# Performance work log

Measured on AMD Instinct MI355X. Metric: run time of the kernel, lower is better.

## Reference

```python
import jax, jax.numpy as jnp
import numpy as np

HID = 512


def _lstm_cell(x, h, c, W_ih, W_hh, b):
    # torch gate order: i, f, g, o ; z: [B, 4H]
    z = x @ W_ih.T + h @ W_hh.T + b
    i, f, g, o = jnp.split(z, 4, axis=-1)
    c_new = jax.nn.sigmoid(f) * c + jax.nn.sigmoid(i) * jnp.tanh(g)
    h_new = jax.nn.sigmoid(o) * jnp.tanh(c_new)
    return h_new, c_new


def setup_inputs() -> dict:
    key = jax.random.key(0)
    ks = jax.random.split(key, 10)
    s = 1.0 / np.sqrt(HID)  # torch default LSTM init scale
    return {
        "inputs": jax.random.normal(ks[0], (512, 512, 1), jnp.float32),
        "targets": jax.random.normal(ks[1], (512, 128, 1), jnp.float32),
        "enc_Wih": jax.random.uniform(ks[2], (4 * HID, 1), jnp.float32, -s, s),
        "enc_Whh": jax.random.uniform(ks[3], (4 * HID, HID), jnp.float32, -s, s),
        "enc_b": jax.random.uniform(ks[4], (4 * HID,), jnp.float32, -s, s),
        "dec_Wih": jax.random.uniform(ks[5], (4 * HID, 1), jnp.float32, -s, s),
        "dec_Whh": jax.random.uniform(ks[6], (4 * HID, HID), jnp.float32, -s, s),
        "dec_b": jax.random.uniform(ks[7], (4 * HID,), jnp.float32, -s, s),
        "lin_W": jax.random.uniform(ks[8], (1, HID), jnp.float32, -s, s),
        "lin_b": jax.random.uniform(ks[9], (1,), jnp.float32, -s, s),
        "target_len": 128,
        "teacher_forcing_ratio": 0,
    }


def reference(inputs, targets, enc_Wih, enc_Whh, enc_b,
              dec_Wih, dec_Whh, dec_b, lin_W, lin_b,
              target_len, teacher_forcing_ratio):
    B = inputs.shape[0]
    H = enc_Whh.shape[1]
    h0 = jnp.zeros((B, H), inputs.dtype)
    c0 = jnp.zeros((B, H), inputs.dtype)

    # ---- encoder: scan over source timesteps ----
    def enc_step(carry, x_t):  # x_t: [B, 1]
        h, c = carry
        h, c = _lstm_cell(x_t, h, c, enc_Wih, enc_Whh, enc_b)
        return (h, c), None

    (h, c), _ = jax.lax.scan(enc_step, (h0, c0), jnp.swapaxes(inputs, 0, 1))

    x0 = inputs[:, -1, :]  # [B, 1]

    def dec_step(carry, _):
        h, c, x = carry
        h, c = _lstm_cell(x, h, c, dec_Wih, dec_Whh, dec_b)
        out = h @ lin_W.T + lin_b  # [B, 1]
        return (h, c, out), out

    _, outs = jax.lax.scan(dec_step, (h, c, x0), None, length=target_len)
    return jnp.swapaxes(outs, 0, 1)  # [B, target_len, 1]
```

## Files before the change

### kernel.cpp

```cpp
#include <hip/hip_runtime.h>
#include <math.h>

#define HID    512
#define BATCH  512
#define TIN    512
#define TOUT   128
#define FOUR_H 2048
#define STEPS  (TIN + TOUT)

typedef __bf16 bf16x8 __attribute__((ext_vector_type(8)));
typedef float floatx4 __attribute__((ext_vector_type(4)));
typedef int   int4v   __attribute__((ext_vector_type(4)));

#define GLOADX4_SC(dst, p) \
    asm volatile("global_load_dwordx4 %0, %1, off sc0 sc1" : "=v"(dst) : "v"(p))
#define GSTOREX4_SC(p, v) \
    asm volatile("global_store_dwordx4 %0, %1, off sc0 sc1" :: "v"(p), "v"(v) : "memory")
#define GLOADX4_C(dst, p) \
    asm volatile("global_load_dwordx4 %0, %1, off" : "=v"(dst) : "v"(p))
#define WAIT_T1(N, r) asm volatile("s_waitcnt vmcnt(" #N ")" : "+v"(r))
#define WAIT_T4(N, B) asm volatile("s_waitcnt vmcnt(" #N ")" \
    : "+v"((B)[0]), "+v"((B)[1]), "+v"((B)[2]), "+v"((B)[3]))

__device__ __forceinline__ float fsig(float x) {
    return __builtin_amdgcn_rcpf(1.0f + __expf(-x));
}
__device__ __forceinline__ float ftanh(float x) {
    return 1.0f - 2.0f * __builtin_amdgcn_rcpf(1.0f + __expf(2.0f * x));
}

__global__ __launch_bounds__(256) void pack_w(
    const float* __restrict__ W, __bf16* __restrict__ Apk)
{
    int tid = blockIdx.x * 256 + threadIdx.x;
    int mp  = tid >> 6;
    int kg  = tid & 63;
    int g   = mp & 3;
    int j   = mp >> 2;
    int r   = g * HID + j;
    int blk   = mp >> 7;
    int rg    = (mp >> 4) & 7;
    int lr    = mp & 15;
    int chunk = kg >> 2;
    int lq    = kg & 3;
    int lane  = lq * 16 + lr;
    const float* src = W + (size_t)r * HID + kg * 8;
    size_t offHi = ((size_t)(((blk * 8 + rg) * 16 + chunk) * 2 + 0) * 512) + lane * 8;
    size_t offLo = ((size_t)(((blk * 8 + rg) * 16 + chunk) * 2 + 1) * 512) + lane * 8;
    __bf16 hibuf[8], lobuf[8];
    #pragma unroll
    for (int i = 0; i < 8; ++i) {
        float x = src[i];
        __bf16 hi = (__bf16)x;
        hibuf[i] = hi;
        lobuf[i] = (__bf16)(x - (float)hi);
    }
    *(bf16x8*)(Apk + offHi) = *(bf16x8*)hibuf;
    *(bf16x8*)(Apk + offLo) = *(bf16x8*)lobuf;
}

__global__ __launch_bounds__(256) void pack_v(
    const float* __restrict__ Wih, const float* __restrict__ b,
    float* __restrict__ WihP, float* __restrict__ bP)
{
    int mp = blockIdx.x * 256 + threadIdx.x;
    int g  = mp & 3;
    int j  = mp >> 2;
    int r  = g * HID + j;
    WihP[mp] = Wih[r];
    bP[mp]   = b[r];
}

__global__ __launch_bounds__(256) void transpose_in(
    const float* __restrict__ in, float* __restrict__ outT)
{
    int idx = blockIdx.x * 256 + threadIdx.x;
    int t = idx >> 9, b = idx & 511;
    outT[idx] = in[(size_t)b * TIN + t];
}

__global__ __launch_bounds__(256, 1) void lstm_persistent(
    const __bf16* __restrict__ ApkEnc,
    const __bf16* __restrict__ ApkDec,
    const float* __restrict__ WihPenc, const float* __restrict__ biasPenc,
    const float* __restrict__ WihPdec, const float* __restrict__ biasPdec,
    const float* __restrict__ inputsT,
    const float* __restrict__ linW, const float* __restrict__ linb,
    __bf16* __restrict__ h0,
    __bf16* __restrict__ h1,
    __bf16* __restrict__ h2,
    float* __restrict__ xacc,
    int* __restrict__ barrier_ws,
    float* __restrict__ out)
{
    extern __shared__ char smem[];
    __bf16* Alds   = (__bf16*)smem;
    char*   Bring  = smem + 131072;
    __bf16* hstage = (__bf16*)(smem + 147456);
    float*  xred   = (float*)(smem + 152576);

    const int tid  = threadIdx.x;
    const int lane = tid & 63;
    const int w    = tid >> 6;
    const int lr   = lane & 15;
    const int lq   = lane >> 4;
    const int by   = blockIdx.x >> 4;
    const int blk  = blockIdx.x & 15;
    const int nbase = by * 32;
    const int rgbase = 2 * w;
    const bool STREAM = (w >= 2);

    int* flagv = barrier_ws;

    const int m0a = blk * 128 + (rgbase + 0) * 16 + lq * 4;
    const int m0b = blk * 128 + (rgbase + 1) * 16 + lq * 4;
    const floatx4 wihE[2] = { *(const floatx4*)(WihPenc + m0a), *(const floatx4*)(WihPenc + m0b) };
    const floatx4 bE[2]   = { *(const floatx4*)(biasPenc + m0a), *(const floatx4*)(biasPenc + m0b) };
    const floatx4 wihD[2] = { *(const floatx4*)(WihPdec + m0a), *(const floatx4*)(WihPdec + m0b) };
    const floatx4 bD[2]   = { *(const floatx4*)(biasPdec + m0a), *(const floatx4*)(biasPdec + m0b) };
    const float lw[2] = { linW[m0a >> 2], linW[m0b >> 2] };
    const float lb = linb[0];

    int bn[2];
    #pragma unroll
    for (int nt = 0; nt < 2; ++nt) bn[nt] = nbase + nt * 16 + lr;

    {
        float* hz = (float*)hstage;
        for (int i = tid; i < 1280; i += 256) hz[i] = 0.f;
    }
    {
        const int4v* srcp = (const int4v*)(ApkEnc + (size_t)blk * 131072);
        int4v* dstp = (int4v*)Alds;
        for (int i = tid; i < 8192; i += 256) dstp[i] = srcp[i];
    }
    __syncthreads();

    float creg[2][2] = {{0.f, 0.f}, {0.f, 0.f}};

    __bf16* hA = h0;
    __bf16* hB = h1;
    __bf16* hC = h2;

    for (int s = 0; s < STEPS; ++s) {
        const bool dec = (s >= TIN);
        const int  t   = s - TIN;
        const __bf16* Acur = dec ? ApkDec : ApkEnc;

        if (s == TIN) {
            const int4v* srcp = (const int4v*)(ApkDec + (size_t)blk * 131072);
            int4v* dstp = (int4v*)Alds;
            for (int i = tid; i < 8192; i += 256) dstp[i] = srcp[i];
            __syncthreads();
        }

        const __bf16* srcB = hA + (size_t)by * 32768 + tid * 8;
        __bf16*       hout = hB;
        const __bf16* Ag   = Acur + (size_t)blk * 131072;

        float xq[2];
        if (!dec) {
            #pragma unroll
            for (int nt = 0; nt < 2; ++nt)
                xq[nt] = inputsT[s * BATCH + bn[nt]];
            asm volatile("" ::: "memory");
        }

        int4v st[4];
        int4v areg[2][4];
        if (STREAM) {
            #pragma unroll
            for (int mb = 0; mb < 2; ++mb)
                #pragma unroll
                for (int pl = 0; pl < 2; ++pl)
                    GLOADX4_C(areg[0][mb * 2 + pl],
                              Ag + (size_t)((((rgbase + mb) * 16 + blk) * 2 + pl) * 512) + lane * 8);
            #pragma unroll
            for (int mb = 0; mb < 2; ++mb)
                #pragma unroll
                for (int pl = 0; pl < 2; ++pl)
                    GLOADX4_C(areg[1][mb * 2 + pl],
                              Ag + (size_t)((((rgbase + mb) * 16 + ((blk + 1) & 15)) * 2 + pl) * 512) + lane * 8);
        }

        if (tid < 16) {
            const int* fp = &flagv[by * 16 + tid];
            while (__hip_atomic_load(fp, __ATOMIC_RELAXED, __HIP_MEMORY_SCOPE_AGENT) < s) {
                __builtin_amdgcn_s_sleep(1);
            }
        }

        floatx4 acc[2][2];
        #pragma unroll
        for (int mb = 0; mb < 2; ++mb)
            #pragma unroll
            for (int nt = 0; nt < 2; ++nt) acc[mb][nt] = floatx4{0.f, 0.f, 0.f, 0.f};

        {
            bf16x8 ah[2], al[2];
            if (STREAM) {
                WAIT_T4(4, areg[0]);
                #pragma unroll
                for (int mb = 0; mb < 2; ++mb) {
                    ah[mb] = __builtin_bit_cast(bf16x8, areg[0][mb * 2 + 0]);
                    al[mb] = __builtin_bit_cast(bf16x8, areg[0][mb * 2 + 1]);
                }
            } else {
                #pragma unroll
                for (int mb = 0; mb < 2; ++mb) {
                    const char* ap = (const char*)Alds
                        + (((rgbase + mb) * 16 + blk) * 2) * 1024 + lane * 16;
                    ah[mb] = *(const bf16x8*)(ap);
                    al[mb] = *(const bf16x8*)(ap + 1024);
                }
            }
            const char* hb = (const char*)hstage;
            const int kq = lane >> 4, lrp = lane & 15;
            bf16x8 bh0 = *(const bf16x8*)(hb + (     lrp) * 80 + kq * 16);
            bf16x8 bl0 = *(const bf16x8*)(hb + (32 + lrp) * 80 + kq * 16);
            bf16x8 bh1 = *(const bf16x8*)(hb + (16 + lrp) * 80 + kq * 16);
            bf16x8 bl1 = *(const bf16x8*)(hb + (48 + lrp) * 80 + kq * 16);
            #pragma unroll
            for (int mb = 0; mb < 2; ++mb) {
                acc[mb][0] = __builtin_amdgcn_mfma_f32_16x16x32_bf16(ah[mb], bh0, acc[mb][0], 0, 0, 0);
                acc[mb][1] = __builtin_amdgcn_mfma_f32_16x16x32_bf16(ah[mb], bh1, acc[mb][1], 0, 0, 0);
                acc[mb][0] = __builtin_amdgcn_mfma_f32_16x16x32_bf16(al[mb], bh0, acc[mb][0], 0, 0, 0);
                acc[mb][1] = __builtin_amdgcn_mfma_f32_16x16x32_bf16(al[mb], bh1, acc[mb][1], 0, 0, 0);
                acc[mb][0] = __builtin_amdgcn_mfma_f32_16x16x32_bf16(ah[mb], bl0, acc[mb][0], 0, 0, 0);
                acc[mb][1] = __builtin_amdgcn_mfma_f32_16x16x32_bf16(ah[mb], bl1, acc[mb][1], 0, 0, 0);
            }
        }

        __syncthreads();

        if (dec) {
            if (tid < 32) xred[tid] = 0.f;
            if (blk == 0) {
                if (t >= 1 && tid < 32) {
                    float v = __hip_atomic_load(&xacc[((t - 1) % 3) * BATCH + nbase + tid],
                                                __ATOMIC_RELAXED, __HIP_MEMORY_SCOPE_AGENT) + lb;
                    out[(size_t)(nbase + tid) * TOUT + (t - 1)] = v;
                }
                if (tid >= 32 && tid < 64) {
                    __hip_atomic_store(&xacc[((t + 1) % 3) * BATCH + nbase + (tid - 32)], 0.0f,
                                       __ATOMIC_RELAXED, __HIP_MEMORY_SCOPE_AGENT);
                }
            }
            #pragma unroll
            for (int nt = 0; nt < 2; ++nt)
                xq[nt] = (t == 0) ? inputsT[(TIN - 1) * BATCH + bn[nt]]
                                  : __hip_atomic_load(&xacc[((t - 1) % 3) * BATCH + bn[nt]],
                                                      __ATOMIC_RELAXED, __HIP_MEMORY_SCOPE_AGENT) + lb;
            asm volatile("" ::: "memory");
        }

        GLOADX4_SC(st[1], srcB + (size_t)((blk + 1) & 15) * 2048);
        GLOADX4_SC(st[2], srcB + (size_t)((blk + 2) & 15) * 2048);
        GLOADX4_SC(st[3], srcB + (size_t)((blk + 3) & 15) * 2048);

        #pragma unroll
        for (int it = 1; it < 16; ++it) {
            const int c = (blk + it) & 15;

            if (STREAM) {
                if      (it == 1)  { WAIT_T1(2,  st[it & 3]); }
                else if (it == 2)  { WAIT_T1(6,  st[it & 3]); }
                else if (it <= 13) { WAIT_T1(10, st[it & 3]); }
                else if (it == 14) { WAIT_T1(9,  st[it & 3]); }
                else               { WAIT_T1(8,  st[it & 3]); }
            } else {
                if      (it <= 13) { WAIT_T1(2, st[it & 3]); }
                else if (it == 14) { WAIT_T1(1, st[it & 3]); }
                else               { WAIT_T1(0, st[it & 3]); }
            }
            *(int4v*)(Bring + (it & 3) * 4096 + tid * 16) = st[it & 3];

            if (STREAM && it + 1 < 16) {
                const int cn = (blk + it + 1) & 15;
                #pragma unroll
                for (int mb = 0; mb < 2; ++mb)
                    #pragma unroll
                    for (int pl = 0; pl < 2; ++pl)
                        GLOADX4_C(areg[(it + 1) & 1][mb * 2 + pl],
                                  Ag + (size_t)((((rgbase + mb) * 16 + cn) * 2 + pl) * 512) + lane * 8);
            }
            if (it + 3 < 16)
                GLOADX4_SC(st[(it + 3) & 3], srcB + (size_t)((blk + it + 3) & 15) * 2048);

            __syncthreads();

            bf16x8 ah[2], al[2];
            if (STREAM) {
                if      (it == 1)  { WAIT_T4(7, areg[1]); }
                else if (it <= 12) { WAIT_T4(6, areg[it & 1]); }
                else if (it == 13) { WAIT_T4(5, areg[1]); }
                else if (it == 14) { WAIT_T4(4, areg[0]); }
                else               { WAIT_T4(0, areg[1]); }
                #pragma unroll
                for (int mb = 0; mb < 2; ++mb) {
                    ah[mb] = __builtin_bit_cast(bf16x8, areg[it & 1][mb * 2 + 0]);
                    al[mb] = __builtin_bit_cast(bf16x8, areg[it & 1][mb * 2 + 1]);
                }
            } else {
                #pragma unroll
                for (int mb = 0; mb < 2; ++mb) {
                    const char* ap = (const char*)Alds
                        + (((rgbase + mb) * 16 + c) * 2) * 1024 + lane * 16;
                    ah[mb] = *(const bf16x8*)(ap);
                    al[mb] = *(const bf16x8*)(ap + 1024);
                }
            }

            const char* bs = Bring + (it & 3) * 4096;
            bf16x8 bh0 = *(const bf16x8*)(bs + (0 * 128 + 0 * 64 + lane) * 16);
            bf16x8 bl0 = *(const bf16x8*)(bs + (0 * 128 + 1 * 64 + lane) * 16);
            bf16x8 bh1 = *(const bf16x8*)(bs + (1 * 128 + 0 * 64 + lane) * 16);
            bf16x8 bl1 = *(const bf16x8*)(bs + (1 * 128 + 1 * 64 + lane) * 16);

            #pragma unroll
            for (int mb = 0; mb < 2; ++mb) {
                acc[mb][0] = __builtin_amdgcn_mfma_f32_16x16x32_bf16(ah[mb], bh0, acc[mb][0], 0, 0, 0);
                acc[mb][1] = __builtin_amdgcn_mfma_f32_16x16x32_bf16(ah[mb], bh1, acc[mb][1], 0, 0, 0);
                acc[mb][0] = __builtin_amdgcn_mfma_f32_16x16x32_bf16(al[mb], bh0, acc[mb][0], 0, 0, 0);
                acc[mb][1] = __builtin_amdgcn_mfma_f32_16x16x32_bf16(al[mb], bh1, acc[mb][1], 0, 0, 0);
                acc[mb][0] = __builtin_amdgcn_mfma_f32_16x16x32_bf16(ah[mb], bl0, acc[mb][0], 0, 0, 0);
                acc[mb][1] = __builtin_amdgcn_mfma_f32_16x16x32_bf16(ah[mb], bl1, acc[mb][1], 0, 0, 0);
            }
        }

        const floatx4* wih = dec ? wihD : wihE;
        const floatx4* bb  = dec ? bD   : bE;
        float px[2] = {0.f, 0.f};
        #pragma unroll
        for (int mb = 0; mb < 2; ++mb) {
            const int jlocal = (rgbase + mb) * 4 + lq;
            #pragma unroll
            for (int nt = 0; nt < 2; ++nt) {
                float x  = xq[nt];
                float i_ = fsig (acc[mb][nt][0] + bb[mb][0] + x * wih[mb][0]);
                float f_ = fsig (acc[mb][nt][1] + bb[mb][1] + x * wih[mb][1]);
                float g_ = ftanh(acc[mb][nt][2] + bb[mb][2] + x * wih[mb][2]);
                float o_ = fsig (acc[mb][nt][3] + bb[mb][3] + x * wih[mb][3]);
                float cv = f_ * creg[mb][nt] + i_ * g_;
                creg[mb][nt] = cv;
                float h  = o_ * ftanh(cv);
                __bf16 hh = (__bf16)h;
                int bl = nt * 16 + lr;
                hstage[bl * 40 + jlocal] = hh;
                hstage[(32 + bl) * 40 + jlocal] = (__bf16)(h - (float)hh);
                if (dec) {
                    float v = h * lw[mb];
                    px[nt] += v;
                }
            }
        }
        if (dec) {
            #pragma unroll
            for (int nt = 0; nt < 2; ++nt) {
                px[nt] += __shfl_xor(px[nt], 16);
                px[nt] += __shfl_xor(px[nt], 32);
            }
        }

        __syncthreads();

        {
            int nt = tid >> 7, pl = (tid >> 6) & 1, ln = tid & 63;
            int kq = ln >> 4, lrp = ln & 15;
            const char* src = (const char*)hstage + (pl * 32 + nt * 16 + lrp) * 80 + kq * 16;
            int4v v = *(const int4v*)src;
            __bf16* dst = hout + (size_t)by * 32768 + blk * 2048 + tid * 8;
            GSTOREX4_SC(dst, v);
        }

        if (dec && lane < 16) {
            #pragma unroll
            for (int nt = 0; nt < 2; ++nt) atomicAdd(&xred[nt * 16 + lr], px[nt]);
        }
        __syncthreads();
        if (dec && tid < 32) {
            atomicAdd(&xacc[(t % 3) * BATCH + nbase + tid], xred[tid]);
        }

        __builtin_amdgcn_s_waitcnt(0);
        __syncthreads();
        if (tid == 0) {
            __hip_atomic_store(&flagv[by * 16 + blk], s + 1,
                               __ATOMIC_RELAXED, __HIP_MEMORY_SCOPE_AGENT);
        }

        __bf16* htmp = hA; hA = hB; hB = hC; hC = htmp;
    }

    if (blk == 0) {
        if (tid < 16) {
            const int* fp = &flagv[by * 16 + tid];
            while (__hip_atomic_load(fp, __ATOMIC_RELAXED, __HIP_MEMORY_SCOPE_AGENT) < STEPS) {
                __builtin_amdgcn_s_sleep(1);
            }
        }
        __syncthreads();
        if (tid < 32) {
            float v = __hip_atomic_load(&xacc[((TOUT - 1) % 3) * BATCH + nbase + tid],
                                        __ATOMIC_RELAXED, __HIP_MEMORY_SCOPE_AGENT) + lb;
            out[(size_t)(nbase + tid) * TOUT + (TOUT - 1)] = v;
        }
    }
}

extern "C" void kernel_launch(void* const* d_in, const int* in_sizes, int n_in,
                              void* d_out, int out_size, void* d_ws, size_t ws_size,
                              hipStream_t stream) {
    const float* inputs  = (const float*)d_in[0];
    const float* enc_Wih = (const float*)d_in[2];
    const float* enc_Whh = (const float*)d_in[3];
    const float* enc_b   = (const float*)d_in[4];
    const float* dec_Wih = (const float*)d_in[5];
    const float* dec_Whh = (const float*)d_in[6];
    const float* dec_b   = (const float*)d_in[7];
    const float* lin_W   = (const float*)d_in[8];
    const float* lin_b   = (const float*)d_in[9];
    float* out = (float*)d_out;

    char* ws = (char*)d_ws;
    const size_t SZ_APK = (size_t)FOUR_H * HID * 2 * sizeof(__bf16);
    const size_t SZ_V   = (size_t)FOUR_H * sizeof(float);
    const size_t SZ_HF  = (size_t)16 * 16 * 256 * 8 * sizeof(__bf16);

    __bf16* ApkEnc = (__bf16*)(ws);
    __bf16* ApkDec = (__bf16*)(ws + SZ_APK);
    char* p = ws + 2 * SZ_APK;
    float* WihPenc  = (float*)p;  p += SZ_V;
    float* biasPenc = (float*)p;  p += SZ_V;
    float* WihPdec  = (float*)p;  p += SZ_V;
    float* biasPdec = (float*)p;  p += SZ_V;
    float* inputsT  = (float*)p;  p += (size_t)TIN * BATCH * sizeof(float);
    __bf16* h0 = (__bf16*)p;      p += SZ_HF;
    __bf16* h1 = (__bf16*)p;      p += SZ_HF;
    __bf16* h2 = (__bf16*)p;      p += SZ_HF;
    float* xacc  = (float*)p;     p += 3 * BATCH * sizeof(float);
    int* barrier_ws = (int*)p;    p += 1024 * sizeof(int);

    pack_w<<<512, 256, 0, stream>>>(enc_Whh, ApkEnc);
    pack_w<<<512, 256, 0, stream>>>(dec_Whh, ApkDec);
    pack_v<<<8, 256, 0, stream>>>(enc_Wih, enc_b, WihPenc, biasPenc);
    pack_v<<<8, 256, 0, stream>>>(dec_Wih, dec_b, WihPdec, biasPdec);
    transpose_in<<<1024, 256, 0, stream>>>(inputs, inputsT);
    hipMemsetAsync(h0, 0, SZ_HF, stream);
    hipMemsetAsync(xacc, 0, 3 * BATCH * sizeof(float), stream);
    hipMemsetAsync(barrier_ws, 0, 1024 * sizeof(int), stream);

    const int shmem = 131072 + 16384 + 5120 + 128;
    hipFuncSetAttribute((const void*)lstm_persistent,
                        hipFuncAttributeMaxDynamicSharedMemorySize, shmem);

    void* args[] = {
        (void*)&ApkEnc, (void*)&ApkDec,
        (void*)&WihPenc, (void*)&biasPenc, (void*)&WihPdec, (void*)&biasPdec,
        (void*)&inputsT, (void*)&lin_W, (void*)&lin_b,
        (void*)&h0, (void*)&h1, (void*)&h2,
        (void*)&xacc, (void*)&barrier_ws, (void*)&out
    };
    hipLaunchCooperativeKernel((void*)lstm_persistent, dim3(256), dim3(256),
                               args, shmem, stream);
}
```

Measured before the change: 5.013 ms.

## Replace per-block flags with counter barrier and prefetch next step's local MFMA

Replaces the per-block step flags (each block waiting on 16 peers' flags) with a single arrive counter per batch group that blocks increment and then spin on. The first chunk of the next step's matrix product, which uses the block's own hidden-state slice already in LDS, is now computed before waiting on the barrier, so it overlaps the wait. The hidden-state buffers drop from triple to double buffering. Double buffering relies on the full barrier for write-after-read safety, and the simplified vmcnt waits must stay correct for the changed load order.

Result: faster. 4.200 ms (-16.2%).

```diff
diff --git a/kernel.cpp b/kernel.cpp
--- a/kernel.cpp
+++ b/kernel.cpp
@@ -88,7 +88,6 @@
     const float* __restrict__ linW, const float* __restrict__ linb,
     __bf16* __restrict__ h0,
     __bf16* __restrict__ h1,
-    __bf16* __restrict__ h2,
     float* __restrict__ xacc,
     int* __restrict__ barrier_ws,
     float* __restrict__ out)
@@ -110,7 +109,7 @@
     const int rgbase = 2 * w;
     const bool STREAM = (w >= 2);
 
-    int* flagv = barrier_ws;
+    int* arrive = barrier_ws + by * 32;
 
     const int m0a = blk * 128 + (rgbase + 0) * 16 + lq * 4;
     const int m0b = blk * 128 + (rgbase + 1) * 16 + lq * 4;
@@ -135,104 +134,77 @@
         for (int i = tid; i < 8192; i += 256) dstp[i] = srcp[i];
     }
     __syncthreads();
+    __builtin_amdgcn_s_waitcnt(0);
 
     float creg[2][2] = {{0.f, 0.f}, {0.f, 0.f}};
 
-    __bf16* hA = h0;
-    __bf16* hB = h1;
-    __bf16* hC = h2;
+    floatx4 acc[2][2];
+    int4v areg[2][4];
+
+    {
+        const __bf16* AgN = ApkEnc + (size_t)blk * 131072;
+        #pragma unroll
+        for (int mb = 0; mb < 2; ++mb)
+            #pragma unroll
+            for (int nt = 0; nt < 2; ++nt) acc[mb][nt] = floatx4{0.f, 0.f, 0.f, 0.f};
+        if (STREAM) {
+            #pragma unroll
+            for (int mb = 0; mb < 2; ++mb)
+                #pragma unroll
+                for (int pl = 0; pl < 2; ++pl)
+                    GLOADX4_C(areg[0][mb * 2 + pl],
+                              AgN + (size_t)((((rgbase + mb) * 16 + blk) * 2 + pl) * 512) + lane * 8);
+            #pragma unroll
+            for (int mb = 0; mb < 2; ++mb)
+                #pragma unroll
+                for (int pl = 0; pl < 2; ++pl)
+                    GLOADX4_C(areg[1][mb * 2 + pl],
+                              AgN + (size_t)((((rgbase + mb) * 16 + ((blk + 1) & 15)) * 2 + pl) * 512) + lane * 8);
+            WAIT_T4(4, areg[0]);
+        }
+        bf16x8 ah[2], al[2];
+        if (STREAM) {
+            #pragma unroll
+            for (int mb = 0; mb < 2; ++mb) {
+                ah[mb] = __builtin_bit_cast(bf16x8, areg[0][mb * 2 + 0]);
+                al[mb] = __builtin_bit_cast(bf16x8, areg[0][mb * 2 + 1]);
+            }
+        } else {
+            #pragma unroll
+            for (int mb = 0; mb < 2; ++mb) {
+                const char* ap = (const char*)Alds + (((rgbase + mb) * 16 + blk) * 2) * 1024 + lane * 16;
+                ah[mb] = *(const bf16x8*)(ap);
+                al[mb] = *(const bf16x8*)(ap + 1024);
+            }
+        }
+        const char* hb = (const char*)hstage;
+        const int kq = lane >> 4, lrp = lane & 15;
+        bf16x8 bh0 = *(const bf16x8*)(hb + (     lrp) * 80 + kq * 16);
+        bf16x8 bl0 = *(const bf16x8*)(hb + (32 + lrp) * 80 + kq * 16);
+        bf16x8 bh1 = *(const bf16x8*)(hb + (16 + lrp) * 80 + kq * 16);
+        bf16x8 bl1 = *(const bf16x8*)(hb + (48 + lrp) * 80 + kq * 16);
+        #pragma unroll
+        for (int mb = 0; mb < 2; ++mb) {
+            acc[mb][0] = __builtin_amdgcn_mfma_f32_16x16x32_bf16(ah[mb], bh0, acc[mb][0], 0, 0, 0);
+            acc[mb][1] = __builtin_amdgcn_mfma_f32_16x16x32_bf16(ah[mb], bh1, acc[mb][1], 0, 0, 0);
+            acc[mb][0] = __builtin_amdgcn_mfma_f32_16x16x32_bf16(al[mb], bh0, acc[mb][0], 0, 0, 0);
+            acc[mb][1] = __builtin_amdgcn_mfma_f32_16x16x32_bf16(al[mb], bh1, acc[mb][1], 0, 0, 0);
+            acc[mb][0] = __builtin_amdgcn_mfma_f32_16x16x32_bf16(ah[mb], bl0, acc[mb][0], 0, 0, 0);
+            acc[mb][1] = __builtin_amdgcn_mfma_f32_16x16x32_bf16(ah[mb], bl1, acc[mb][1], 0, 0, 0);
+        }
+    }
 
     for (int s = 0; s < STEPS; ++s) {
         const bool dec = (s >= TIN);
         const int  t   = s - TIN;
         const __bf16* Acur = dec ? ApkDec : ApkEnc;
 
-        if (s == TIN) {
-            const int4v* srcp = (const int4v*)(ApkDec + (size_t)blk * 131072);
-            int4v* dstp = (int4v*)Alds;
-            for (int i = tid; i < 8192; i += 256) dstp[i] = srcp[i];
-            __syncthreads();
-        }
-
-        const __bf16* srcB = hA + (size_t)by * 32768 + tid * 8;
-        __bf16*       hout = hB;
+        const __bf16* hin  = (s & 1) ? h1 : h0;
+        __bf16*       hout = (s & 1) ? h0 : h1;
+        const __bf16* srcB = hin + (size_t)by * 32768 + tid * 8;
         const __bf16* Ag   = Acur + (size_t)blk * 131072;
 
         float xq[2];
-        if (!dec) {
-            #pragma unroll
-            for (int nt = 0; nt < 2; ++nt)
-                xq[nt] = inputsT[s * BATCH + bn[nt]];
-            asm volatile("" ::: "memory");
-        }
-
-        int4v st[4];
-        int4v areg[2][4];
-        if (STREAM) {
-            #pragma unroll
-            for (int mb = 0; mb < 2; ++mb)
-                #pragma unroll
-                for (int pl = 0; pl < 2; ++pl)
-                    GLOADX4_C(areg[0][mb * 2 + pl],
-                              Ag + (size_t)((((rgbase + mb) * 16 + blk) * 2 + pl) * 512) + lane * 8);
-            #pragma unroll
-            for (int mb = 0; mb < 2; ++mb)
-                #pragma unroll
-                for (int pl = 0; pl < 2; ++pl)
-                    GLOADX4_C(areg[1][mb * 2 + pl],
-                              Ag + (size_t)((((rgbase + mb) * 16 + ((blk + 1) & 15)) * 2 + pl) * 512) + lane * 8);
-        }
-
-        if (tid < 16) {
-            const int* fp = &flagv[by * 16 + tid];
-            while (__hip_atomic_load(fp, __ATOMIC_RELAXED, __HIP_MEMORY_SCOPE_AGENT) < s) {
-                __builtin_amdgcn_s_sleep(1);
-            }
-        }
-
-        floatx4 acc[2][2];
-        #pragma unroll
-        for (int mb = 0; mb < 2; ++mb)
-            #pragma unroll
-            for (int nt = 0; nt < 2; ++nt) acc[mb][nt] = floatx4{0.f, 0.f, 0.f, 0.f};
-
-        {
-            bf16x8 ah[2], al[2];
-            if (STREAM) {
-                WAIT_T4(4, areg[0]);
-                #pragma unroll
-                for (int mb = 0; mb < 2; ++mb) {
-                    ah[mb] = __builtin_bit_cast(bf16x8, areg[0][mb * 2 + 0]);
-                    al[mb] = __builtin_bit_cast(bf16x8, areg[0][mb * 2 + 1]);
-                }
-            } else {
-                #pragma unroll
-                for (int mb = 0; mb < 2; ++mb) {
-                    const char* ap = (const char*)Alds
-                        + (((rgbase + mb) * 16 + blk) * 2) * 1024 + lane * 16;
-                    ah[mb] = *(const bf16x8*)(ap);
-                    al[mb] = *(const bf16x8*)(ap + 1024);
-                }
-            }
-            const char* hb = (const char*)hstage;
-            const int kq = lane >> 4, lrp = lane & 15;
-            bf16x8 bh0 = *(const bf16x8*)(hb + (     lrp) * 80 + kq * 16);
-            bf16x8 bl0 = *(const bf16x8*)(hb + (32 + lrp) * 80 + kq * 16);
-            bf16x8 bh1 = *(const bf16x8*)(hb + (16 + lrp) * 80 + kq * 16);
-            bf16x8 bl1 = *(const bf16x8*)(hb + (48 + lrp) * 80 + kq * 16);
-            #pragma unroll
-            for (int mb = 0; mb < 2; ++mb) {
-                acc[mb][0] = __builtin_amdgcn_mfma_f32_16x16x32_bf16(ah[mb], bh0, acc[mb][0], 0, 0, 0);
-                acc[mb][1] = __builtin_amdgcn_mfma_f32_16x16x32_bf16(ah[mb], bh1, acc[mb][1], 0, 0, 0);
-                acc[mb][0] = __builtin_amdgcn_mfma_f32_16x16x32_bf16(al[mb], bh0, acc[mb][0], 0, 0, 0);
-                acc[mb][1] = __builtin_amdgcn_mfma_f32_16x16x32_bf16(al[mb], bh1, acc[mb][1], 0, 0, 0);
-                acc[mb][0] = __builtin_amdgcn_mfma_f32_16x16x32_bf16(ah[mb], bl0, acc[mb][0], 0, 0, 0);
-                acc[mb][1] = __builtin_amdgcn_mfma_f32_16x16x32_bf16(ah[mb], bl1, acc[mb][1], 0, 0, 0);
-            }
-        }
-
-        __syncthreads();
-
         if (dec) {
             if (tid < 32) xred[tid] = 0.f;
             if (blk == 0) {
@@ -251,9 +223,14 @@
                 xq[nt] = (t == 0) ? inputsT[(TIN - 1) * BATCH + bn[nt]]
                                   : __hip_atomic_load(&xacc[((t - 1) % 3) * BATCH + bn[nt]],
                                                       __ATOMIC_RELAXED, __HIP_MEMORY_SCOPE_AGENT) + lb;
-            asm volatile("" ::: "memory");
-        }
-
+        } else {
+            #pragma unroll
+            for (int nt = 0; nt < 2; ++nt)
+                xq[nt] = inputsT[s * BATCH + bn[nt]];
+        }
+        asm volatile("" ::: "memory");
+
+        int4v st[4];
         GLOADX4_SC(st[1], srcB + (size_t)((blk + 1) & 15) * 2048);
         GLOADX4_SC(st[2], srcB + (size_t)((blk + 2) & 15) * 2048);
         GLOADX4_SC(st[3], srcB + (size_t)((blk + 3) & 15) * 2048);
@@ -263,11 +240,8 @@
             const int c = (blk + it) & 15;
 
             if (STREAM) {
-                if      (it == 1)  { WAIT_T1(2,  st[it & 3]); }
-                else if (it == 2)  { WAIT_T1(6,  st[it & 3]); }
-                else if (it <= 13) { WAIT_T1(10, st[it & 3]); }
-                else if (it == 14) { WAIT_T1(9,  st[it & 3]); }
-                else               { WAIT_T1(8,  st[it & 3]); }
+                if      (it == 1) { WAIT_T1(2, st[1]); }
+                else if (it == 2) { WAIT_T1(6, st[2]); }
             } else {
                 if      (it <= 13) { WAIT_T1(2, st[it & 3]); }
                 else if (it == 14) { WAIT_T1(1, st[it & 3]); }
@@ -291,7 +265,7 @@
 
             bf16x8 ah[2], al[2];
             if (STREAM) {
-                if      (it == 1)  { WAIT_T4(7, areg[1]); }
+                if      (it == 1)  {  }
                 else if (it <= 12) { WAIT_T4(6, areg[it & 1]); }
                 else if (it == 13) { WAIT_T4(5, areg[1]); }
                 else if (it == 14) { WAIT_T4(4, areg[0]); }
@@ -385,26 +359,85 @@
         __builtin_amdgcn_s_waitcnt(0);
         __syncthreads();
         if (tid == 0) {
-            __hip_atomic_store(&flagv[by * 16 + blk], s + 1,
-                               __ATOMIC_RELAXED, __HIP_MEMORY_SCOPE_AGENT);
-        }
-
-        __bf16* htmp = hA; hA = hB; hB = hC; hC = htmp;
-    }
-
-    if (blk == 0) {
-        if (tid < 16) {
-            const int* fp = &flagv[by * 16 + tid];
-            while (__hip_atomic_load(fp, __ATOMIC_RELAXED, __HIP_MEMORY_SCOPE_AGENT) < STEPS) {
-                __builtin_amdgcn_s_sleep(1);
-            }
+            (void)__hip_atomic_fetch_add(arrive, 1, __ATOMIC_RELAXED, __HIP_MEMORY_SCOPE_AGENT);
+        }
+
+        if (s + 1 == TIN) {
+            const int4v* srcp = (const int4v*)(ApkDec + (size_t)blk * 131072);
+            int4v* dstp = (int4v*)Alds;
+            for (int i = tid; i < 8192; i += 256) dstp[i] = srcp[i];
+            __syncthreads();
+            __builtin_amdgcn_s_waitcnt(0);
+        }
+        if (s + 1 < STEPS) {
+            const __bf16* AgN = ((s + 1 >= TIN) ? ApkDec : ApkEnc) + (size_t)blk * 131072;
+            #pragma unroll
+            for (int mb = 0; mb < 2; ++mb)
+                #pragma unroll
+                for (int nt = 0; nt < 2; ++nt) acc[mb][nt] = floatx4{0.f, 0.f, 0.f, 0.f};
+            if (STREAM) {
+                #pragma unroll
+                for (int mb = 0; mb < 2; ++mb)
+                    #pragma unroll
+                    for (int pl = 0; pl < 2; ++pl)
+                        GLOADX4_C(areg[0][mb * 2 + pl],
+                                  AgN + (size_t)((((rgbase + mb) * 16 + blk) * 2 + pl) * 512) + lane * 8);
+                #pragma unroll
+                for (int mb = 0; mb < 2; ++mb)
+                    #pragma unroll
+                    for (int pl = 0; pl < 2; ++pl)
+                        GLOADX4_C(areg[1][mb * 2 + pl],
+                                  AgN + (size_t)((((rgbase + mb) * 16 + ((blk + 1) & 15)) * 2 + pl) * 512) + lane * 8);
+                WAIT_T4(4, areg[0]);
+            }
+            bf16x8 ah[2], al[2];
+            if (STREAM) {
+                #pragma unroll
+                for (int mb = 0; mb < 2; ++mb) {
+                    ah[mb] = __builtin_bit_cast(bf16x8, areg[0][mb * 2 + 0]);
+                    al[mb] = __builtin_bit_cast(bf16x8, areg[0][mb * 2 + 1]);
+                }
+            } else {
+                #pragma unroll
+                for (int mb = 0; mb < 2; ++mb) {
+                    const char* ap = (const char*)Alds + (((rgbase + mb) * 16 + blk) * 2) * 1024 + lane * 16;
+                    ah[mb] = *(const bf16x8*)(ap);
+                    al[mb] = *(const bf16x8*)(ap + 1024);
+                }
+            }
+            const char* hb = (const char*)hstage;
+            const int kq = lane >> 4, lrp = lane & 15;
+            bf16x8 bh0 = *(const bf16x8*)(hb + (     lrp) * 80 + kq * 16);
+            bf16x8 bl0 = *(const bf16x8*)(hb + (32 + lrp) * 80 + kq * 16);
+            bf16x8 bh1 = *(const bf16x8*)(hb + (16 + lrp) * 80 + kq * 16);
+            bf16x8 bl1 = *(const bf16x8*)(hb + (48 + lrp) * 80 + kq * 16);
+            #pragma unroll
+            for (int mb = 0; mb < 2; ++mb) {
+                acc[mb][0] = __builtin_amdgcn_mfma_f32_16x16x32_bf16(ah[mb], bh0, acc[mb][0], 0, 0, 0);
+                acc[mb][1] = __builtin_amdgcn_mfma_f32_16x16x32_bf16(ah[mb], bh1, acc[mb][1], 0, 0, 0);
+                acc[mb][0] = __builtin_amdgcn_mfma_f32_16x16x32_bf16(al[mb], bh0, acc[mb][0], 0, 0, 0);
+                acc[mb][1] = __builtin_amdgcn_mfma_f32_16x16x32_bf16(al[mb], bh1, acc[mb][1], 0, 0, 0);
+                acc[mb][0] = __builtin_amdgcn_mfma_f32_16x16x32_bf16(ah[mb], bl0, acc[mb][0], 0, 0, 0);
+                acc[mb][1] = __builtin_amdgcn_mfma_f32_16x16x32_bf16(ah[mb], bl1, acc[mb][1], 0, 0, 0);
+            }
+        }
+
+        if (tid == 0) {
+            int target = 16 * (s + 1);
+            int n;
+            do {
+                n = __hip_atomic_load(arrive, __ATOMIC_RELAXED, __HIP_MEMORY_SCOPE_AGENT);
+                if (n >= target) break;
+                __builtin_amdgcn_s_sleep(2);
+            } while (1);
         }
         __syncthreads();
-        if (tid < 32) {
-            float v = __hip_atomic_load(&xacc[((TOUT - 1) % 3) * BATCH + nbase + tid],
-                                        __ATOMIC_RELAXED, __HIP_MEMORY_SCOPE_AGENT) + lb;
-            out[(size_t)(nbase + tid) * TOUT + (TOUT - 1)] = v;
-        }
+    }
+
+    if (blk == 0 && tid < 32) {
+        float v = __hip_atomic_load(&xacc[((TOUT - 1) % 3) * BATCH + nbase + tid],
+                                    __ATOMIC_RELAXED, __HIP_MEMORY_SCOPE_AGENT) + lb;
+        out[(size_t)(nbase + tid) * TOUT + (TOUT - 1)] = v;
     }
 }
 
@@ -437,7 +470,6 @@
     float* inputsT  = (float*)p;  p += (size_t)TIN * BATCH * sizeof(float);
     __bf16* h0 = (__bf16*)p;      p += SZ_HF;
     __bf16* h1 = (__bf16*)p;      p += SZ_HF;
-    __bf16* h2 = (__bf16*)p;      p += SZ_HF;
     float* xacc  = (float*)p;     p += 3 * BATCH * sizeof(float);
     int* barrier_ws = (int*)p;    p += 1024 * sizeof(int);
 
@@ -458,7 +490,7 @@
         (void*)&ApkEnc, (void*)&ApkDec,
         (void*)&WihPenc, (void*)&biasPenc, (void*)&WihPdec, (void*)&biasPdec,
         (void*)&inputsT, (void*)&lin_W, (void*)&lin_b,
-        (void*)&h0, (void*)&h1, (void*)&h2,
+        (void*)&h0, (void*)&h1,
         (void*)&xacc, (void*)&barrier_ws, (void*)&out
     };
     hipLaunchCooperativeKernel((void*)lstm_persistent, dim3(256), dim3(256),
```
